# Optimization experiments

Hardware: AMD Instinct MI355X
Metric: run time of the kernel (lower is better)

The kernel has to match this reference:

```python
import math
import jax, jax.numpy as jnp
import numpy as np

MODEL_DIM = 4096
NUM_EXPERTS = 64
NUM_TOKENS = 8192
CAPACITY_FACTOR = 1.0


def setup_inputs() -> dict:
    key = jax.random.key(0)
    kx, kw = jax.random.split(key)
    x = jax.random.normal(kx, (NUM_TOKENS, MODEL_DIM), dtype=jnp.float32)
    # nn.Linear weight: [num_experts, model_dim]
    W = jax.random.normal(kw, (NUM_EXPERTS, MODEL_DIM), dtype=jnp.float32) * (1.0 / math.sqrt(MODEL_DIM))
    return {"x": x, "W": W}


def reference(x, W):
    # gating projection (no bias), cast to fp32 as in top1gating
    logits = jnp.matmul(x, W.T).astype(jnp.float32)  # [S, E]
    num_tokens, num_experts = logits.shape
    capacity = int(CAPACITY_FACTOR * math.ceil(num_tokens / num_experts))

    indices1_s = jnp.argmax(logits, axis=1)                        # [S]
    gates = jax.nn.softmax(logits, axis=1)                         # [S, E]
    mask1 = jax.nn.one_hot(indices1_s, num_experts, dtype=jnp.float32)  # [S, E]
    gates1_s = jnp.sum(gates * mask1, axis=1)                      # [S]
    # per-expert running position of each routed token
    locations1 = jnp.cumsum(mask1, axis=0) - 1.0                   # [S, E]
    locations1_s = jnp.sum(locations1 * mask1, axis=1)             # [S]

    return (indices1_s.astype(jnp.int32),
            capacity,
            locations1_s.astype(jnp.int32),
            gates1_s,
            num_experts)
```

## Files before the change

### kernel.cpp

```cpp
#include <hip/hip_runtime.h>
#include <math.h>

#define NTOK 8192
#define MDIM 4096
#define NEXP 64
#define CAPACITY 128.0f

#define OFF_IDX  0
#define OFF_CAP  8192
#define OFF_LOC  8193
#define OFF_GATE 16385
#define OFF_NE   24577

#define NSLICE 16
#define KSL    (MDIM / NSLICE)
#define KC     32
#define NCH    (KSL / KC)

#define WS_CNT_OFF  0
#define WS_RK_OFF   16384
#define WS_PART_OFF 24576

using bf16x8 = __attribute__((ext_vector_type(8))) short;
using f32x4  = __attribute__((ext_vector_type(4))) float;
typedef unsigned int u32;

static __device__ __forceinline__ u32 cvtpk(float a0, float a1) {
    u32 r;
    asm("v_cvt_pk_bf16_f32 %0, %1, %2" : "=v"(r) : "v"(a0), "v"(a1));
    return r;
}

static __device__ __forceinline__ void split2(
    float a0, float a1, u32& p1, u32& p2, u32& p3)
{
    p1 = cvtpk(a0, a1);
    float t0 = a0 - __uint_as_float(p1 << 16);
    float t1 = a1 - __uint_as_float(p1 & 0xffff0000u);
    p2 = cvtpk(t0, t1);
    float u0 = t0 - __uint_as_float(p2 << 16);
    float u1 = t1 - __uint_as_float(p2 & 0xffff0000u);
    p3 = cvtpk(u0, u1);
}

__global__ __launch_bounds__(512, 4) void gate_mfma(
    const float* __restrict__ x,
    const float* __restrict__ W,
    float* __restrict__ part)
{
    __shared__ __align__(16) unsigned short wl[12][64][32];
    __shared__ __align__(16) float4 xs[8][32][8];

    const int tid   = threadIdx.x;
    const int lane  = tid & 63;
    const int wv    = tid >> 6;
    const int m     = lane & 15;
    const int g     = lane >> 4;
    const int tok0  = blockIdx.x * 256 + wv * 32;
    const int slice = blockIdx.y;
    const int k0    = slice * KSL;

    const float4* __restrict__ x4 = (const float4*)x;

    auto stage = [&](int c) {
        #pragma unroll
        for (int j = 0; j < 4; ++j) {
            const int row  = j * 8 + (lane >> 3);
            const int srcs = (lane & 7) ^ (row & 7);
            const float4* gsrc = x4 + (size_t)(tok0 + row) * (MDIM / 4)
                                 + (k0 >> 2) + c * 8 + srcs;
            void* ldst = (void*)&xs[wv][j * 8][0];
            __builtin_amdgcn_global_load_lds(
                (const __attribute__((address_space(1))) void*)gsrc,
                (__attribute__((address_space(3))) void*)ldst, 16, 0, 0);
        }
    };

    auto splitW = [&](int h) {
        #pragma unroll
        for (int r = 0; r < 4; ++r) {
            const int j4  = r * 512 + tid;
            const int e   = j4 >> 5;
            const int kk4 = j4 & 31;
            float4 v = *(const float4*)(W + (size_t)e * MDIM + k0 + h * 128 + kk4 * 4);
            const int c4    = kk4 >> 3;
            const int slog  = (kk4 >> 1) & 3;
            const int half16 = kk4 & 1;
            const int phys  = slog ^ ((e >> 1) & 3);
            u32 w1a, w2a, w3a, w1b, w2b, w3b;
            split2(v.x, v.y, w1a, w2a, w3a);
            split2(v.z, v.w, w1b, w2b, w3b);
            *(uint2*)&wl[c4 * 3 + 0][e][phys * 8 + half16 * 4] = make_uint2(w1a, w1b);
            *(uint2*)&wl[c4 * 3 + 1][e][phys * 8 + half16 * 4] = make_uint2(w2a, w2b);
            *(uint2*)&wl[c4 * 3 + 2][e][phys * 8 + half16 * 4] = make_uint2(w3a, w3b);
        }
    };

    auto cvt = [&](float4 lo, float4 hi, bf16x8& r0, bf16x8& r1, bf16x8& r2) {
        union { u32 u[4]; bf16x8 v; } P1, P2, P3;
        split2(lo.x, lo.y, P1.u[0], P2.u[0], P3.u[0]);
        split2(lo.z, lo.w, P1.u[1], P2.u[1], P3.u[1]);
        split2(hi.x, hi.y, P1.u[2], P2.u[2], P3.u[2]);
        split2(hi.z, hi.w, P1.u[3], P2.u[3], P3.u[3]);
        r0 = P1.v; r1 = P2.v; r2 = P3.v;
    };

    f32x4 acc[2][4];
    #pragma unroll
    for (int gr = 0; gr < 2; ++gr)
        #pragma unroll
        for (int nt = 0; nt < 4; ++nt) acc[gr][nt] = (f32x4){0.f, 0.f, 0.f, 0.f};

    stage(0);

    for (int h = 0; h < 2; ++h) {
        if (h) __syncthreads();
        splitW(h);
        __syncthreads();

        #pragma unroll
        for (int c4 = 0; c4 < 4; ++c4) {
            const int c = h * 4 + c4;

            bf16x8 w[3][4];
            #pragma unroll
            for (int t = 0; t < 3; ++t)
                #pragma unroll
                for (int nt = 0; nt < 4; ++nt) {
                    const int e    = nt * 16 + m;
                    const int phys = g ^ ((e >> 1) & 3);
                    w[t][nt] = *(const bf16x8*)&wl[c4 * 3 + t][e][phys * 8];
                }

            bf16x8 a[2][3];
            #pragma unroll
            for (int gr = 0; gr < 2; ++gr) {
                const int row = gr * 16 + m;
                float4 lo = xs[wv][row][(2 * g    ) ^ (m & 7)];
                float4 hi = xs[wv][row][(2 * g + 1) ^ (m & 7)];
                cvt(lo, hi, a[gr][0], a[gr][1], a[gr][2]);
            }

            __builtin_amdgcn_sched_barrier(0);
            if (c + 1 < NCH) stage(c + 1);

            #pragma unroll
            for (int gr = 0; gr < 2; ++gr)
                #pragma unroll
                for (int nt = 0; nt < 4; ++nt)
                    acc[gr][nt] = __builtin_amdgcn_mfma_f32_16x16x32_bf16(a[gr][2], w[0][nt], acc[gr][nt], 0, 0, 0);
            #pragma unroll
            for (int gr = 0; gr < 2; ++gr)
                #pragma unroll
                for (int nt = 0; nt < 4; ++nt)
                    acc[gr][nt] = __builtin_amdgcn_mfma_f32_16x16x32_bf16(a[gr][0], w[2][nt], acc[gr][nt], 0, 0, 0);
            #pragma unroll
            for (int gr = 0; gr < 2; ++gr)
                #pragma unroll
                for (int nt = 0; nt < 4; ++nt)
                    acc[gr][nt] = __builtin_amdgcn_mfma_f32_16x16x32_bf16(a[gr][1], w[1][nt], acc[gr][nt], 0, 0, 0);
            #pragma unroll
            for (int gr = 0; gr < 2; ++gr)
                #pragma unroll
                for (int nt = 0; nt < 4; ++nt)
                    acc[gr][nt] = __builtin_amdgcn_mfma_f32_16x16x32_bf16(a[gr][1], w[0][nt], acc[gr][nt], 0, 0, 0);
            #pragma unroll
            for (int gr = 0; gr < 2; ++gr)
                #pragma unroll
                for (int nt = 0; nt < 4; ++nt)
                    acc[gr][nt] = __builtin_amdgcn_mfma_f32_16x16x32_bf16(a[gr][0], w[1][nt], acc[gr][nt], 0, 0, 0);
            #pragma unroll
            for (int gr = 0; gr < 2; ++gr)
                #pragma unroll
                for (int nt = 0; nt < 4; ++nt)
                    acc[gr][nt] = __builtin_amdgcn_mfma_f32_16x16x32_bf16(a[gr][0], w[0][nt], acc[gr][nt], 0, 0, 0);
        }
    }

    #pragma unroll
    for (int gr = 0; gr < 2; ++gr)
        #pragma unroll
        for (int nt = 0; nt < 4; ++nt)
            #pragma unroll
            for (int r = 0; r < 4; ++r) {
                const int tokr = tok0 + gr * 16 + g * 4 + r;
                part[((size_t)slice * NTOK + tokr) * 64 + nt * 16 + m] = acc[gr][nt][r];
            }
}

template<int S>
__global__ __launch_bounds__(256) void reduce_count(
    const float* __restrict__ part,
    float* __restrict__ out,
    int* __restrict__ cnt,
    int* __restrict__ rk)
{
    __shared__ int eidx[32];

    const int tid  = threadIdx.x;
    const int tok0 = blockIdx.x * 32;
    const int trel = tid >> 3;
    const int tok  = tok0 + trel;
    const int q    = tid & 7;

    const float4* __restrict__ p4 = (const float4*)part;

    float4 a[2];
    #pragma unroll
    for (int r = 0; r < 2; ++r) a[r] = make_float4(0.f, 0.f, 0.f, 0.f);
    for (int s = 0; s < S; ++s) {
        #pragma unroll
        for (int r = 0; r < 2; ++r) {
            float4 v = p4[((size_t)s * NTOK + tok) * 16 + q * 2 + r];
            a[r].x += v.x; a[r].y += v.y; a[r].z += v.z; a[r].w += v.w;
        }
    }

    float vals[8] = {a[0].x, a[0].y, a[0].z, a[0].w,
                     a[1].x, a[1].y, a[1].z, a[1].w};

    float bm = vals[0];
    int   be = q * 8;
    #pragma unroll
    for (int j = 1; j < 8; ++j)
        if (vals[j] > bm) { bm = vals[j]; be = q * 8 + j; }
    #pragma unroll
    for (int off = 1; off <= 4; off <<= 1) {
        float om = __shfl_xor(bm, off, 64);
        int   oe = __shfl_xor(be, off, 64);
        if (om > bm || (om == bm && oe < be)) { bm = om; be = oe; }
    }

    float es = 0.f;
    #pragma unroll
    for (int j = 0; j < 8; ++j) es += expf(vals[j] - bm);
    #pragma unroll
    for (int off = 1; off <= 4; off <<= 1)
        es += __shfl_xor(es, off, 64);

    if (q == 0) {
        out[OFF_IDX  + tok] = (float)be;
        out[OFF_GATE + tok] = 1.0f / es;
        eidx[trel] = be;
    }
    __syncthreads();

    if (tid < 64) {
        const int e = (tid < 32) ? eidx[tid] : -1;
        const unsigned long long lt =
            (tid == 0) ? 0ull : ((~0ull) >> (64 - tid));
        unsigned long long mymask = 0;
        int myrk = 0;
        for (int ee = 0; ee < 64; ++ee) {
            unsigned long long mb = __ballot(e == ee);
            if (tid == ee) mymask = mb;
            if (e == ee)   myrk   = (int)__popcll(mb & lt);
        }
        cnt[blockIdx.x * 64 + tid] = (int)__popcll(mymask);
        if (tid < 32) rk[tok0 + tid] = myrk;
    }
    if (tid == 0 && blockIdx.x == 0) {
        out[OFF_CAP] = CAPACITY;
        out[OFF_NE]  = (float)NEXP;
    }
}

__global__ __launch_bounds__(512) void scan_emit(
    const float* __restrict__ idxf,
    const int* __restrict__ cnt,
    const int* __restrict__ rk,
    float* __restrict__ out)
{
    __shared__ int sc[256][64];
    __shared__ int ps[64][8];

    const int tid = threadIdx.x;
    const int e   = tid >> 3;
    const int q   = tid & 7;

    #pragma unroll
    for (int r = 0; r < 32; ++r) sc[0][r * 512 + tid] = cnt[r * 512 + tid];
    __syncthreads();

    {
        int sum = 0;
        #pragma unroll
        for (int j = 0; j < 32; ++j) sum += sc[q * 32 + j][e];
        ps[e][q] = sum;
    }
    __syncthreads();

    {
        int base = 0;
        for (int qq = 0; qq < 8; ++qq) { if (qq < q) base += ps[e][qq]; }
        #pragma unroll
        for (int j = 0; j < 32; ++j) {
            int ch = q * 32 + j;
            int v  = sc[ch][e];
            sc[ch][e] = base;
            base += v;
        }
    }
    __syncthreads();

    #pragma unroll
    for (int r = 0; r < 16; ++r) {
        const int s  = r * 512 + tid;
        const int ee = (int)idxf[s];
        out[OFF_LOC + s] = (float)(sc[s >> 5][ee] + rk[s]);
    }
}

extern "C" void kernel_launch(void* const* d_in, const int* in_sizes, int n_in,
                              void* d_out, int out_size, void* d_ws, size_t ws_size,
                              hipStream_t stream)
{
    const float* x = (const float*)d_in[0];
    const float* W = (const float*)d_in[1];
    float* out = (float*)d_out;

    int*   cnt  = (int*)d_ws + WS_CNT_OFF;
    int*   rk   = (int*)d_ws + WS_RK_OFF;
    float* part = (float*)d_ws + WS_PART_OFF;

    gate_mfma<<<dim3(32, NSLICE), 512, 0, stream>>>(x, W, part);
    reduce_count<NSLICE><<<256, 256, 0, stream>>>(part, out, cnt, rk);
    scan_emit<<<1, 512, 0, stream>>>(out + OFF_IDX, cnt, rk, out);
}
```

Before: 231.5 us.

## Load x directly into registers with double buffering instead of LDS staging

Drops the per-wave LDS staging of x tiles done with global_load_lds. Each lane now reads its MFMA operand fragments straight from global memory into registers, using two register buffers that prefetch two chunks ahead. The h loop is fully unrolled so the buffer choice resolves at compile time. This removes LDS traffic and frees 32 KB of shared memory, which can help occupancy, but adds VGPR pressure and leaves the global reads less coalesced.

```diff
diff --git a/kernel.cpp b/kernel.cpp
--- a/kernel.cpp
+++ b/kernel.cpp
@@ -49,7 +49,6 @@
     float* __restrict__ part)
 {
     __shared__ __align__(16) unsigned short wl[12][64][32];
-    __shared__ __align__(16) float4 xs[8][32][8];
 
     const int tid   = threadIdx.x;
     const int lane  = tid & 63;
@@ -60,20 +59,14 @@
     const int slice = blockIdx.y;
     const int k0    = slice * KSL;
 
-    const float4* __restrict__ x4 = (const float4*)x;
-
-    auto stage = [&](int c) {
-        #pragma unroll
-        for (int j = 0; j < 4; ++j) {
-            const int row  = j * 8 + (lane >> 3);
-            const int srcs = (lane & 7) ^ (row & 7);
-            const float4* gsrc = x4 + (size_t)(tok0 + row) * (MDIM / 4)
-                                 + (k0 >> 2) + c * 8 + srcs;
-            void* ldst = (void*)&xs[wv][j * 8][0];
-            __builtin_amdgcn_global_load_lds(
-                (const __attribute__((address_space(1))) void*)gsrc,
-                (__attribute__((address_space(3))) void*)ldst, 16, 0, 0);
-        }
+    const float* __restrict__ xp = x + (size_t)(tok0 + m) * MDIM + k0 + g * 8;
+
+    auto loadx = [&](int c, float4* d) {
+        const float* p = xp + c * KC;
+        d[0] = *(const float4*)(p);
+        d[1] = *(const float4*)(p + 4);
+        d[2] = *(const float4*)(p + 16 * MDIM);
+        d[3] = *(const float4*)(p + 16 * MDIM + 4);
     };
 
     auto splitW = [&](int h) {
@@ -83,10 +76,10 @@
             const int e   = j4 >> 5;
             const int kk4 = j4 & 31;
             float4 v = *(const float4*)(W + (size_t)e * MDIM + k0 + h * 128 + kk4 * 4);
-            const int c4    = kk4 >> 3;
-            const int slog  = (kk4 >> 1) & 3;
+            const int c4     = kk4 >> 3;
+            const int slog   = (kk4 >> 1) & 3;
             const int half16 = kk4 & 1;
-            const int phys  = slog ^ ((e >> 1) & 3);
+            const int phys   = slog ^ ((e >> 1) & 3);
             u32 w1a, w2a, w3a, w1b, w2b, w3b;
             split2(v.x, v.y, w1a, w2a, w3a);
             split2(v.z, v.w, w1b, w2b, w3b);
@@ -111,8 +104,11 @@
         #pragma unroll
         for (int nt = 0; nt < 4; ++nt) acc[gr][nt] = (f32x4){0.f, 0.f, 0.f, 0.f};
 
-    stage(0);
-
+    float4 bufA[4], bufB[4];
+    loadx(0, bufA);
+    loadx(1, bufB);
+
+    #pragma unroll
     for (int h = 0; h < 2; ++h) {
         if (h) __syncthreads();
         splitW(h);
@@ -121,6 +117,7 @@
         #pragma unroll
         for (int c4 = 0; c4 < 4; ++c4) {
             const int c = h * 4 + c4;
+            float4* buf = (c & 1) ? bufB : bufA;
 
             bf16x8 w[3][4];
             #pragma unroll
@@ -133,16 +130,10 @@
                 }
 
             bf16x8 a[2][3];
-            #pragma unroll
-            for (int gr = 0; gr < 2; ++gr) {
-                const int row = gr * 16 + m;
-                float4 lo = xs[wv][row][(2 * g    ) ^ (m & 7)];
-                float4 hi = xs[wv][row][(2 * g + 1) ^ (m & 7)];
-                cvt(lo, hi, a[gr][0], a[gr][1], a[gr][2]);
-            }
-
-            __builtin_amdgcn_sched_barrier(0);
-            if (c + 1 < NCH) stage(c + 1);
+            cvt(buf[0], buf[1], a[0][0], a[0][1], a[0][2]);
+            cvt(buf[2], buf[3], a[1][0], a[1][1], a[1][2]);
+
+            if (c + 2 < NCH) loadx(c + 2, buf);
 
             #pragma unroll
             for (int gr = 0; gr < 2; ++gr)
```

After: 232.3 us. Within noise of the previous version (+0.4%).
